# Kernel optimization log

Measured on AMD Instinct MI355X. Metric: run time of the kernel, lower is better.

Reference implementation:

```python
import jax, jax.numpy as jnp
import numpy as np

# Static layer configuration (from init_kwargs)
C_IN, H, W = 8, 32, 32
C_OUT, KH, KW = 16, 3, 3
SH, SW = 1, 1
PH, PW = 1, 1
OH = (H + 2 * PH - KH) // SH + 1
OW = (W + 2 * PW - KW) // SW + 1
N_IN = C_IN * H * W      # 8192 input-layer neurons
N_OUT = C_OUT * OH * OW  # 16384 output-layer neurons


def setup_inputs() -> dict:
    key = jax.random.key(0)
    k1, k2, k3, k4 = jax.random.split(key, 4)
    base = jax.random.normal(k1, (C_IN, H, W), dtype=jnp.float32)
    rad = jax.random.uniform(k2, (C_IN, H, W), dtype=jnp.float32)
    return {
        "concrete_lower": base - rad,   # ensure lower <= upper
        "concrete_upper": base + rad,
        "weights": jax.random.normal(k3, (C_OUT, C_IN, KH, KW), dtype=jnp.float32) * 0.1,
        "bias": jax.random.normal(k4, (C_OUT,), dtype=jnp.float32) * 0.1,
    }


def build_abstract_matrix(weights, bias):
    """Vectorized equivalent of _create_conv2d_channel_v0 over all channels.

    Produces M of shape (N_IN+1, N_OUT+1): column (c*OH*OW + i*OW + j) holds the
    affine coefficients (over flattened input neurons, bias in last row) of
    output pixel (c, i, j); last column is the homogeneous [0...0, 1] column.
    """
    idy = jnp.arange(OH)[:, None] * SH - PH + jnp.arange(KH)[None, :]  # (OH, KH)
    idx = jnp.arange(OW)[:, None] * SW - PW + jnp.arange(KW)[None, :]  # (OW, KW)
    valid = (((idy >= 0) & (idy < H))[:, :, None, None]
             & ((idx >= 0) & (idx < W))[None, None, :, :])             # (OH, KH, OW, KW)

    cin = jnp.arange(C_IN)
    # broadcast layout: (C_OUT, C_IN, OH, KH, OW, KW)
    rows = (cin[None, :, None, None, None, None] * (H * W)
            + idy[None, None, :, :, None, None] * W
            + idx[None, None, None, None, :, :])
    oc = jnp.arange(C_OUT)
    cols = (oc[:, None, None, None, None, None] * (OH * OW)
            + jnp.arange(OH)[None, None, :, None, None, None] * OW
            + jnp.arange(OW)[None, None, None, None, :, None])
    vals = weights[:, :, None, :, None, :]  # (C_OUT, C_IN, 1, KH, 1, KW)

    shape = (C_OUT, C_IN, OH, KH, OW, KW)
    rows_b = jnp.broadcast_to(rows, shape).reshape(-1)
    cols_b = jnp.broadcast_to(cols, shape).reshape(-1)
    vals_b = jnp.broadcast_to(vals, shape).reshape(-1)
    valid_b = jnp.broadcast_to(valid[None, None], shape).reshape(-1)
    # padding taps (out of input bounds) -> out-of-range row index, dropped by scatter
    rows_b = jnp.where(valid_b, rows_b, N_IN + 1)

    M = jnp.zeros((N_IN + 1, N_OUT + 1), dtype=jnp.float32)
    M = M.at[rows_b, cols_b].set(vals_b, mode="drop")
    M = M.at[N_IN, :N_OUT].set(jnp.repeat(bias, OH * OW))  # bias row per output pixel
    M = M.at[N_IN, N_OUT].set(1.0)                          # homogeneous corner
    return M


def back_substitute(M, l_in, u_in, lower=True):
    # Interval evaluation of the affine map: positive coeffs pair with one bound,
    # negative with the other; last row of M is the bias.
    Wc = M[:-1, :]
    b = M[-1, :]
    pos = jnp.maximum(Wc, 0.0)
    neg = jnp.minimum(Wc, 0.0)
    if lower:
        return l_in @ pos + u_in @ neg + b
    return u_in @ pos + l_in @ neg + b


def reference(concrete_lower, concrete_upper, weights, bias):
    M = build_abstract_matrix(weights, bias)  # abstract lower == upper for a conv layer
    l = concrete_lower.reshape(-1)
    u = concrete_upper.reshape(-1)
    lo = back_substitute(M, l, u, lower=True)[:N_OUT].reshape(C_OUT, OH, OW)
    hi = back_substitute(M, l, u, lower=False)[:N_OUT].reshape(C_OUT, OH, OW)
    return (lo, hi, M)
```

## Files before the change

kernel.cpp:

```cpp
#include <hip/hip_runtime.h>

#define C_IN  8
#define H     32
#define W     32
#define C_OUT 16
#define KH    3
#define KW    3
#define OH    32
#define OW    32
#define N_IN  (C_IN * H * W)
#define N_OUT (C_OUT * OH * OW)
#define MROWS (N_IN + 1)
#define MCOLS (N_OUT + 1)

typedef float v4f __attribute__((ext_vector_type(4)));

#define NB_SCATTER 4608
#define NB_BIAS    16
#define NB_BOUNDS  64

__global__ __launch_bounds__(256) void scatter_kernel(const float* __restrict__ l_in,
                                                      const float* __restrict__ u_in,
                                                      const float* __restrict__ wts,
                                                      const float* __restrict__ bias,
                                                      float* __restrict__ out,
                                                      float* __restrict__ M) {
    const int b = blockIdx.x;
    const int t = threadIdx.x;

    if (b < NB_SCATTER) {
        const int tid = (b << 8) + t;
        const int r   = tid / 144;
        const int k   = tid - r * 144;
        const int oc  = k / 9;
        const int q   = k - oc * 9;
        const int di  = q / 3;
        const int dj  = q - di * 3;

        const int cin = r >> 10;
        const int iy  = (r >> 5) & 31;
        const int ix  = r & 31;

        const int i = iy - 1 + di;
        const int j = ix - 1 + dj;

        if (((unsigned)i < 32u) & ((unsigned)j < 32u)) {
            const int kh = 2 - di;
            const int kw = 2 - dj;
            const float w = wts[oc * 72 + cin * 9 + kh * 3 + kw];
            M[(size_t)r * MCOLS + (oc << 10) + (i << 5) + j] = w;
        }
        return;
    }

    if (b < NB_SCATTER + NB_BIAS) {
        const int bb = b - NB_SCATTER;
        float* __restrict__ Mrow = M + (size_t)N_IN * MCOLS;
        const float bv = bias[bb];
        v4f v = {bv, bv, bv, bv};
        *(v4f*)(Mrow + (bb << 10) + 4 * t) = v;
        if (bb == 0 && t == 0) Mrow[N_OUT] = 1.0f;
        return;
    }

    int tid = (b - (NB_SCATTER + NB_BIAS)) * 256 + t;
    int c = tid >> 10;
    int i = (tid >> 5) & 31;
    int j = tid & 31;

    float lo = bias[c];
    float hi = lo;

    #pragma unroll
    for (int cin = 0; cin < C_IN; ++cin) {
        #pragma unroll
        for (int kh = 0; kh < KH; ++kh) {
            int iy = i - 1 + kh;
            if ((unsigned)iy >= (unsigned)H) continue;
            #pragma unroll
            for (int kw = 0; kw < KW; ++kw) {
                int ix = j - 1 + kw;
                if ((unsigned)ix >= (unsigned)W) continue;
                float w = wts[c * 72 + cin * 9 + kh * 3 + kw];
                int   r = cin * 1024 + iy * 32 + ix;
                float a  = w * l_in[r];
                float bb = w * u_in[r];
                lo += fminf(a, bb);
                hi += fmaxf(a, bb);
            }
        }
    }
    out[tid]         = lo;
    out[N_OUT + tid] = hi;
}

extern "C" void kernel_launch(void* const* d_in, const int* in_sizes, int n_in,
                              void* d_out, int out_size, void* d_ws, size_t ws_size,
                              hipStream_t stream) {
    const float* lower = (const float*)d_in[0];
    const float* upper = (const float*)d_in[1];
    const float* wts   = (const float*)d_in[2];
    const float* bias  = (const float*)d_in[3];

    float* out = (float*)d_out;
    float* M   = out + 2 * N_OUT;

    hipMemsetAsync(M, 0, (size_t)MROWS * MCOLS * sizeof(float), stream);

    const int grid = NB_SCATTER + NB_BIAS + NB_BOUNDS;
    hipLaunchKernelGGL(scatter_kernel, dim3(grid), dim3(256), 0, stream,
                       lower, upper, wts, bias, out, M);
}
```

Before: 579.9 us.

## Fuse memset into per-row kernel blocks that zero then scatter weights

```diff
diff --git a/kernel.cpp b/kernel.cpp
--- a/kernel.cpp
+++ b/kernel.cpp
@@ -15,55 +15,82 @@
 
 typedef float v4f __attribute__((ext_vector_type(4)));
 
-#define NB_SCATTER 4608
-#define NB_BIAS    16
-#define NB_BOUNDS  64
+#define NB_PRE   65
+#define NB_ROWS  8192
 
-__global__ __launch_bounds__(256) void scatter_kernel(const float* __restrict__ l_in,
-                                                      const float* __restrict__ u_in,
-                                                      const float* __restrict__ wts,
-                                                      const float* __restrict__ bias,
-                                                      float* __restrict__ out,
-                                                      float* __restrict__ M) {
+__global__ __launch_bounds__(256) void fused_kernel(const float* __restrict__ l_in,
+                                                    const float* __restrict__ u_in,
+                                                    const float* __restrict__ wts,
+                                                    const float* __restrict__ bias,
+                                                    float* __restrict__ out,
+                                                    float* __restrict__ M) {
     const int b = blockIdx.x;
     const int t = threadIdx.x;
 
-    if (b < NB_SCATTER) {
-        const int tid = (b << 8) + t;
-        const int r   = tid / 144;
-        const int k   = tid - r * 144;
-        const int oc  = k / 9;
-        const int q   = k - oc * 9;
-        const int di  = q / 3;
-        const int dj  = q - di * 3;
+    if (b >= NB_PRE) {
+        const int r = b - NB_PRE;
+        const size_t base = (size_t)r * MCOLS;
+        float* __restrict__ rowp = M + base;
 
-        const int cin = r >> 10;
         const int iy  = (r >> 5) & 31;
         const int ix  = r & 31;
+        const int cin = r >> 10;
+        bool   ok = false;
+        float  wv = 0.0f;
+        int    col = 0;
+        if (t < 144) {
+            const int oc = t / 9;
+            const int q  = t - oc * 9;
+            const int di = q / 3;
+            const int dj = q - di * 3;
+            const int i  = iy - 1 + di;
+            const int j  = ix - 1 + dj;
+            ok = ((unsigned)i < 32u) & ((unsigned)j < 32u);
+            if (ok) {
+                const int kh = 2 - di;
+                const int kw = 2 - dj;
+                wv  = wts[oc * 72 + cin * 9 + kh * 3 + kw];
+                col = (oc << 10) + (i << 5) + j;
+            }
+        }
 
-        const int i = iy - 1 + di;
-        const int j = ix - 1 + dj;
+        const int mis = (int)(base & 3);
+        const int a   = (4 - mis) & 3;
+        if (t < a) rowp[t] = 0.0f;
 
-        if (((unsigned)i < 32u) & ((unsigned)j < 32u)) {
-            const int kh = 2 - di;
-            const int kw = 2 - dj;
-            const float w = wts[oc * 72 + cin * 9 + kh * 3 + kw];
-            M[(size_t)r * MCOLS + (oc << 10) + (i << 5) + j] = w;
-        }
+        const int nwords = MCOLS - a;
+        const int nspans = nwords >> 2;
+        const int ntail  = nwords & 3;
+        float* __restrict__ bodyp = rowp + a;
+        const v4f zero = {0.0f, 0.0f, 0.0f, 0.0f};
+
+        #pragma unroll
+        for (int k = 0; k < 15; ++k)
+            *(v4f*)(bodyp + 4 * (t + 256 * k)) = zero;
+        if (t + 3840 < nspans)
+            *(v4f*)(bodyp + 4 * (t + 3840)) = zero;
+
+        if (t < ntail) bodyp[4 * nspans + t] = 0.0f;
+
+        __syncthreads();
+
+        if (ok) rowp[col] = wv;
         return;
     }
 
-    if (b < NB_SCATTER + NB_BIAS) {
-        const int bb = b - NB_SCATTER;
+    if (b == 0) {
         float* __restrict__ Mrow = M + (size_t)N_IN * MCOLS;
-        const float bv = bias[bb];
-        v4f v = {bv, bv, bv, bv};
-        *(v4f*)(Mrow + (bb << 10) + 4 * t) = v;
-        if (bb == 0 && t == 0) Mrow[N_OUT] = 1.0f;
+        #pragma unroll
+        for (int k = 0; k < 16; ++k) {
+            const float bv = bias[k];
+            v4f v = {bv, bv, bv, bv};
+            *(v4f*)(Mrow + (k << 10) + 4 * t) = v;
+        }
+        if (t == 0) Mrow[N_OUT] = 1.0f;
         return;
     }
 
-    int tid = (b - (NB_SCATTER + NB_BIAS)) * 256 + t;
+    int tid = (b - 1) * 256 + t;
     int c = tid >> 10;
     int i = (tid >> 5) & 31;
     int j = tid & 31;
@@ -105,9 +132,7 @@
     float* out = (float*)d_out;
     float* M   = out + 2 * N_OUT;
 
-    hipMemsetAsync(M, 0, (size_t)MROWS * MCOLS * sizeof(float), stream);
-
-    const int grid = NB_SCATTER + NB_BIAS + NB_BOUNDS;
-    hipLaunchKernelGGL(scatter_kernel, dim3(grid), dim3(256), 0, stream,
+    const int grid = NB_PRE + NB_ROWS;
+    hipLaunchKernelGGL(fused_kernel, dim3(grid), dim3(256), 0, stream,
                        lower, upper, wts, bias, out, M);
 }
```

New measurement: 545.6 us, median of 2. -5.9%, faster.
